# Kernel tuning notes

Measured on AMD Instinct MI355X. Metric: run time of the kernel, lower is better.

## Reference

```python
import jax, jax.numpy as jnp
import numpy as np

ALPHA = 32.0
RANK = 256
SCALE = ALPHA / RANK


def setup_inputs() -> dict:
    key = jax.random.key(0)
    k1, k2, k3, k4 = jax.random.split(key, 4)
    x = jax.random.normal(k1, (4, 2048, 4096), dtype=jnp.float32)
    A = jax.random.normal(k2, (256, 4096), dtype=jnp.float32)   # (rank, in)
    B = jax.random.normal(k3, (4096, 256), dtype=jnp.float32)   # (out, rank)
    d_A = jnp.ones((256,), dtype=jnp.float32)                    # init = ones (as in module)
    d_B = jax.random.normal(k4, (4096,), dtype=jnp.float32)      # perturbed for a nontrivial test
    return {"x": x, "A": A, "B": B, "d_A": d_A, "d_B": d_B}


def reference(x, A, B, d_A, d_B):
    # Effective weight: diag(d_B) @ B @ diag(d_A) @ A  -> (out, in)
    scaled_A = d_A[:, None] * A                 # (rank, in)
    BA = B @ scaled_A                            # (out, in)
    W_vera = d_B[:, None] * BA                   # (out, in)
    # out = x @ W_vera.T * scale  -> (..., out)
    return jnp.einsum('bsi,oi->bso', x, W_vera) * SCALE
```

## Files before the change

### kernel.cpp

```cpp
#include <hip/hip_runtime.h>
#include <hip/hip_bf16.h>


#define SCALE_F 0.125f
#define M_TOT 8192
#define K_IN 4096
#define RANK 256
#define N_OUT 4096
#define S_SPLIT 4
#define KC 1024

typedef __bf16 bf16_t;
typedef __bf16 bf16x8 __attribute__((ext_vector_type(8)));
typedef __bf16 bf16x4 __attribute__((ext_vector_type(4)));
typedef float f32x4 __attribute__((ext_vector_type(4)));

typedef __attribute__((address_space(3))) unsigned int lds_u32_t;
typedef const __attribute__((address_space(1))) unsigned int glob_u32_t;

__device__ __forceinline__ void async16(const void* g, void* l) {
    __builtin_amdgcn_global_load_lds((glob_u32_t*)g, (lds_u32_t*)l, 16, 0, 0);
}

__global__ __launch_bounds__(256) void conv_A(const float* __restrict__ A,
                                              const float* __restrict__ dA,
                                              bf16_t* __restrict__ Ab) {
    int idx = blockIdx.x * 256 + threadIdx.x;
    float4 v = ((const float4*)A)[idx];
    float s = dA[idx >> 10];
    bf16x4 o;
    o.x = (bf16_t)(v.x * s); o.y = (bf16_t)(v.y * s);
    o.z = (bf16_t)(v.z * s); o.w = (bf16_t)(v.w * s);
    ((bf16x4*)Ab)[idx] = o;
}

__global__ __launch_bounds__(256) void conv_B(const float* __restrict__ B,
                                              bf16_t* __restrict__ Bb) {
    int idx = blockIdx.x * 256 + threadIdx.x;
    float4 v = ((const float4*)B)[idx];
    bf16x4 o;
    o.x = (bf16_t)v.x; o.y = (bf16_t)v.y; o.z = (bf16_t)v.z; o.w = (bf16_t)v.w;
    ((bf16x4*)Bb)[idx] = o;
}

__global__ __launch_bounds__(256) void gemm1(const float* __restrict__ x,
                                             const bf16_t* __restrict__ Ab,
                                             bf16_t* __restrict__ part) {
    __shared__ float  sX[64 * 64];
    __shared__ bf16_t sA[128 * 64];
    const int tid = threadIdx.x;
    const int lane = tid & 63, wave = tid >> 6;
    const int wm = wave >> 1, wn = wave & 1;
    const int l15 = lane & 15, quad = lane >> 4;
    const int bm = blockIdx.x * 64;
    const int bn = blockIdx.y * 128;
    const int k0 = blockIdx.z * KC;

    f32x4 acc[2][4];
    const f32x4 zero = {0.f, 0.f, 0.f, 0.f};
    #pragma unroll
    for (int i = 0; i < 2; i++)
        #pragma unroll
        for (int j = 0; j < 4; j++) acc[i][j] = zero;

    for (int kt = 0; kt < KC; kt += 64) {
        #pragma unroll
        for (int c = 0; c < 4; c++) {
            int idx = c * 256 + tid;
            int m = idx >> 4, kc = (idx & 15) * 4;
            async16(&x[(size_t)(bm + m) * K_IN + k0 + kt + kc], &sX[idx * 4]);
        }
        #pragma unroll
        for (int c = 0; c < 4; c++) {
            int idx = c * 256 + tid;
            int n = idx >> 3, kc = (idx & 7) * 8;
            async16(&Ab[(size_t)(bn + n) * K_IN + k0 + kt + kc], &sA[idx * 8]);
        }
        __syncthreads();
        #pragma unroll
        for (int ks = 0; ks < 2; ks++) {
            bf16x8 af[2], bfr[4];
            #pragma unroll
            for (int i = 0; i < 2; i++) {
                const float* p = &sX[(wm * 32 + i * 16 + l15) * 64 + ks * 32 + quad * 8];
                f32x4 v0 = *(const f32x4*)p;
                f32x4 v1 = *(const f32x4*)(p + 4);
                bf16x8 t;
                t[0] = (bf16_t)v0[0]; t[1] = (bf16_t)v0[1];
                t[2] = (bf16_t)v0[2]; t[3] = (bf16_t)v0[3];
                t[4] = (bf16_t)v1[0]; t[5] = (bf16_t)v1[1];
                t[6] = (bf16_t)v1[2]; t[7] = (bf16_t)v1[3];
                af[i] = t;
            }
            #pragma unroll
            for (int j = 0; j < 4; j++)
                bfr[j] = *(const bf16x8*)&sA[(wn * 64 + j * 16 + l15) * 64 + ks * 32 + quad * 8];
            #pragma unroll
            for (int i = 0; i < 2; i++)
                #pragma unroll
                for (int j = 0; j < 4; j++)
                    acc[i][j] = __builtin_amdgcn_mfma_f32_16x16x32_bf16(af[i], bfr[j], acc[i][j], 0, 0, 0);
        }
        __syncthreads();
    }
    bf16_t* p = part + (size_t)blockIdx.z * M_TOT * RANK;
    #pragma unroll
    for (int i = 0; i < 2; i++) {
        #pragma unroll
        for (int j = 0; j < 4; j++) {
            int col = bn + wn * 64 + j * 16 + l15;
            #pragma unroll
            for (int r = 0; r < 4; r++) {
                int row = bm + wm * 32 + i * 16 + quad * 4 + r;
                p[(size_t)row * RANK + col] = (bf16_t)acc[i][j][r];
            }
        }
    }
}

__global__ __launch_bounds__(256) void reduce_t(const bf16_t* __restrict__ part,
                                                bf16_t* __restrict__ t) {
    int i = (blockIdx.x * 256 + threadIdx.x) * 8;
    float s[8] = {0.f, 0.f, 0.f, 0.f, 0.f, 0.f, 0.f, 0.f};
    #pragma unroll
    for (int z = 0; z < S_SPLIT; z++) {
        bf16x8 v = *(const bf16x8*)&part[(size_t)z * M_TOT * RANK + i];
        #pragma unroll
        for (int e = 0; e < 8; e++) s[e] += (float)v[e];
    }
    bf16x8 o;
    #pragma unroll
    for (int e = 0; e < 8; e++) o[e] = (bf16_t)s[e];
    *(bf16x8*)&t[i] = o;
}

__global__ __launch_bounds__(256) void gemm2(const bf16_t* __restrict__ t,
                                             const bf16_t* __restrict__ Bb,
                                             const float* __restrict__ dB,
                                             float* __restrict__ out) {
    __shared__ bf16_t sT[128 * 64];
    __shared__ bf16_t sB[64 * 64];
    const int tid = threadIdx.x;
    const int lane = tid & 63, wave = tid >> 6;
    const int wm = wave >> 1, wn = wave & 1;
    const int l15 = lane & 15, quad = lane >> 4;
    const int bm = blockIdx.x * 128;
    const int bn = blockIdx.y * 64;

    f32x4 acc[4][2];
    const f32x4 zero = {0.f, 0.f, 0.f, 0.f};
    #pragma unroll
    for (int i = 0; i < 4; i++)
        #pragma unroll
        for (int j = 0; j < 2; j++) acc[i][j] = zero;

    for (int kt = 0; kt < RANK; kt += 64) {
        #pragma unroll
        for (int c = 0; c < 4; c++) {
            int idx = c * 256 + tid;
            int m = idx >> 3, kc = (idx & 7) * 8;
            async16(&t[(size_t)(bm + m) * RANK + kt + kc], &sT[idx * 8]);
        }
        #pragma unroll
        for (int c = 0; c < 2; c++) {
            int idx = c * 256 + tid;
            int n = idx >> 3, kc = (idx & 7) * 8;
            async16(&Bb[(size_t)(bn + n) * RANK + kt + kc], &sB[idx * 8]);
        }
        __syncthreads();
        #pragma unroll
        for (int ks = 0; ks < 2; ks++) {
            bf16x8 af[4], bfr[2];
            #pragma unroll
            for (int i = 0; i < 4; i++)
                af[i] = *(const bf16x8*)&sT[(wm * 64 + i * 16 + l15) * 64 + ks * 32 + quad * 8];
            #pragma unroll
            for (int j = 0; j < 2; j++)
                bfr[j] = *(const bf16x8*)&sB[(wn * 32 + j * 16 + l15) * 64 + ks * 32 + quad * 8];
            #pragma unroll
            for (int i = 0; i < 4; i++)
                #pragma unroll
                for (int j = 0; j < 2; j++)
                    acc[i][j] = __builtin_amdgcn_mfma_f32_16x16x32_bf16(af[i], bfr[j], acc[i][j], 0, 0, 0);
        }
        __syncthreads();
    }
    #pragma unroll
    for (int j = 0; j < 2; j++) {
        int col = bn + wn * 32 + j * 16 + l15;
        float db = dB[col] * SCALE_F;
        #pragma unroll
        for (int i = 0; i < 4; i++) {
            #pragma unroll
            for (int r = 0; r < 4; r++) {
                int row = bm + wm * 64 + i * 16 + quad * 4 + r;
                out[(size_t)row * N_OUT + col] = db * acc[i][j][r];
            }
        }
    }
}

extern "C" void kernel_launch(void* const* d_in, const int* in_sizes, int n_in,
                              void* d_out, int out_size, void* d_ws, size_t ws_size,
                              hipStream_t stream) {
    const float* x  = (const float*)d_in[0];
    const float* A  = (const float*)d_in[1];
    const float* B  = (const float*)d_in[2];
    const float* dA = (const float*)d_in[3];
    const float* dB = (const float*)d_in[4];
    float* out = (float*)d_out;

    char* ws = (char*)d_ws;
    bf16_t* Ab   = (bf16_t*)ws;
    bf16_t* Bb   = (bf16_t*)(ws + (1u << 21));
    bf16_t* tt   = (bf16_t*)(ws + (1u << 22));
    bf16_t* part = (bf16_t*)(ws + (1u << 23));

    conv_A<<<1024, 256, 0, stream>>>(A, dA, Ab);
    conv_B<<<1024, 256, 0, stream>>>(B, Bb);
    gemm1<<<dim3(128, 2, S_SPLIT), 256, 0, stream>>>(x, Ab, part);
    reduce_t<<<1024, 256, 0, stream>>>(part, tt);
    gemm2<<<dim3(64, 64), 256, 0, stream>>>(tt, Bb, dB, out);
}
```

Measured before the change: 314.3 us.

## Retile both GEMMs with XOR-swizzled LDS, full-rank tiles, and merged conversion kernel

Merges the A and B fp32-to-bf16 conversion kernels into one launch. gemm1 now computes all 256 rank columns per block, so x is read from HBM once instead of twice, and it uses split-K 8 with K-step 32. gemm2 drops to 64x64 tiles for more blocks. Both kernels gain XOR swizzles on LDS to avoid bank conflicts. The trade-offs are a doubled partial-sum buffer and reduction traffic, plus higher register pressure in gemm1 with 16 accumulators.

Result: slower. 330.8 us (+5.3%).

```diff
diff --git a/kernel.cpp b/kernel.cpp
--- a/kernel.cpp
+++ b/kernel.cpp
@@ -7,8 +7,8 @@
 #define K_IN 4096
 #define RANK 256
 #define N_OUT 4096
-#define S_SPLIT 4
-#define KC 1024
+#define S_SPLIT 8
+#define KC 512
 
 typedef __bf16 bf16_t;
 typedef __bf16 bf16x8 __attribute__((ext_vector_type(8)));
@@ -22,97 +22,100 @@
     __builtin_amdgcn_global_load_lds((glob_u32_t*)g, (lds_u32_t*)l, 16, 0, 0);
 }
 
-__global__ __launch_bounds__(256) void conv_A(const float* __restrict__ A,
-                                              const float* __restrict__ dA,
-                                              bf16_t* __restrict__ Ab) {
-    int idx = blockIdx.x * 256 + threadIdx.x;
-    float4 v = ((const float4*)A)[idx];
-    float s = dA[idx >> 10];
-    bf16x4 o;
-    o.x = (bf16_t)(v.x * s); o.y = (bf16_t)(v.y * s);
-    o.z = (bf16_t)(v.z * s); o.w = (bf16_t)(v.w * s);
-    ((bf16x4*)Ab)[idx] = o;
-}
-
-__global__ __launch_bounds__(256) void conv_B(const float* __restrict__ B,
-                                              bf16_t* __restrict__ Bb) {
-    int idx = blockIdx.x * 256 + threadIdx.x;
-    float4 v = ((const float4*)B)[idx];
-    bf16x4 o;
-    o.x = (bf16_t)v.x; o.y = (bf16_t)v.y; o.z = (bf16_t)v.z; o.w = (bf16_t)v.w;
-    ((bf16x4*)Bb)[idx] = o;
+__global__ __launch_bounds__(256) void conv_AB(const float* __restrict__ A,
+                                               const float* __restrict__ dA,
+                                               const float* __restrict__ B,
+                                               bf16_t* __restrict__ Ab,
+                                               bf16_t* __restrict__ Bb) {
+    int b = blockIdx.x;
+    int idx = (b & 1023) * 256 + threadIdx.x;
+    if (b < 1024) {
+        float4 v = ((const float4*)A)[idx];
+        float s = dA[idx >> 10];
+        bf16x4 o;
+        o.x = (bf16_t)(v.x * s); o.y = (bf16_t)(v.y * s);
+        o.z = (bf16_t)(v.z * s); o.w = (bf16_t)(v.w * s);
+        ((bf16x4*)Ab)[idx] = o;
+    } else {
+        float4 v = ((const float4*)B)[idx];
+        bf16x4 o;
+        o.x = (bf16_t)v.x; o.y = (bf16_t)v.y; o.z = (bf16_t)v.z; o.w = (bf16_t)v.w;
+        ((bf16x4*)Bb)[idx] = o;
+    }
 }
 
 __global__ __launch_bounds__(256) void gemm1(const float* __restrict__ x,
                                              const bf16_t* __restrict__ Ab,
                                              bf16_t* __restrict__ part) {
-    __shared__ float  sX[64 * 64];
-    __shared__ bf16_t sA[128 * 64];
+    __shared__ float  sX[64 * 32];
+    __shared__ bf16_t sA[256 * 32];
     const int tid = threadIdx.x;
     const int lane = tid & 63, wave = tid >> 6;
     const int wm = wave >> 1, wn = wave & 1;
     const int l15 = lane & 15, quad = lane >> 4;
     const int bm = blockIdx.x * 64;
-    const int bn = blockIdx.y * 128;
-    const int k0 = blockIdx.z * KC;
-
-    f32x4 acc[2][4];
+    const int k0 = blockIdx.y * KC;
+
+    f32x4 acc[2][8];
     const f32x4 zero = {0.f, 0.f, 0.f, 0.f};
     #pragma unroll
     for (int i = 0; i < 2; i++)
         #pragma unroll
-        for (int j = 0; j < 4; j++) acc[i][j] = zero;
-
-    for (int kt = 0; kt < KC; kt += 64) {
+        for (int j = 0; j < 8; j++) acc[i][j] = zero;
+
+    for (int kt = 0; kt < KC; kt += 32) {
+        #pragma unroll
+        for (int c = 0; c < 2; c++) {
+            int u = c * 256 + tid;
+            int m = u >> 3, p = u & 7;
+            int kcu = p ^ (m & 7);
+            async16(&x[(size_t)(bm + m) * K_IN + k0 + kt + kcu * 4], &sX[u * 4]);
+        }
         #pragma unroll
         for (int c = 0; c < 4; c++) {
-            int idx = c * 256 + tid;
-            int m = idx >> 4, kc = (idx & 15) * 4;
-            async16(&x[(size_t)(bm + m) * K_IN + k0 + kt + kc], &sX[idx * 4]);
-        }
-        #pragma unroll
-        for (int c = 0; c < 4; c++) {
-            int idx = c * 256 + tid;
-            int n = idx >> 3, kc = (idx & 7) * 8;
-            async16(&Ab[(size_t)(bn + n) * K_IN + k0 + kt + kc], &sA[idx * 8]);
-        }
-        __syncthreads();
-        #pragma unroll
-        for (int ks = 0; ks < 2; ks++) {
-            bf16x8 af[2], bfr[4];
-            #pragma unroll
-            for (int i = 0; i < 2; i++) {
-                const float* p = &sX[(wm * 32 + i * 16 + l15) * 64 + ks * 32 + quad * 8];
-                f32x4 v0 = *(const f32x4*)p;
-                f32x4 v1 = *(const f32x4*)(p + 4);
-                bf16x8 t;
-                t[0] = (bf16_t)v0[0]; t[1] = (bf16_t)v0[1];
-                t[2] = (bf16_t)v0[2]; t[3] = (bf16_t)v0[3];
-                t[4] = (bf16_t)v1[0]; t[5] = (bf16_t)v1[1];
-                t[6] = (bf16_t)v1[2]; t[7] = (bf16_t)v1[3];
-                af[i] = t;
-            }
-            #pragma unroll
-            for (int j = 0; j < 4; j++)
-                bfr[j] = *(const bf16x8*)&sA[(wn * 64 + j * 16 + l15) * 64 + ks * 32 + quad * 8];
-            #pragma unroll
-            for (int i = 0; i < 2; i++)
-                #pragma unroll
-                for (int j = 0; j < 4; j++)
-                    acc[i][j] = __builtin_amdgcn_mfma_f32_16x16x32_bf16(af[i], bfr[j], acc[i][j], 0, 0, 0);
-        }
-        __syncthreads();
-    }
-    bf16_t* p = part + (size_t)blockIdx.z * M_TOT * RANK;
+            int u = c * 256 + tid;
+            int n = u >> 2, p = u & 3;
+            int kc8 = p ^ ((n >> 1) & 3);
+            async16(&Ab[(size_t)n * K_IN + k0 + kt + kc8 * 8], &sA[u * 8]);
+        }
+        __syncthreads();
+        bf16x8 af[2], bfr[8];
+        #pragma unroll
+        for (int i = 0; i < 2; i++) {
+            int m = wm * 32 + i * 16 + l15;
+            int p0 = (quad * 2) ^ (m & 7);
+            f32x4 v0 = *(const f32x4*)&sX[m * 32 + p0 * 4];
+            f32x4 v1 = *(const f32x4*)&sX[m * 32 + (p0 ^ 1) * 4];
+            bf16x8 t;
+            t[0] = (bf16_t)v0[0]; t[1] = (bf16_t)v0[1];
+            t[2] = (bf16_t)v0[2]; t[3] = (bf16_t)v0[3];
+            t[4] = (bf16_t)v1[0]; t[5] = (bf16_t)v1[1];
+            t[6] = (bf16_t)v1[2]; t[7] = (bf16_t)v1[3];
+            af[i] = t;
+        }
+        #pragma unroll
+        for (int j = 0; j < 8; j++) {
+            int n = wn * 128 + j * 16 + l15;
+            int p = quad ^ ((n >> 1) & 3);
+            bfr[j] = *(const bf16x8*)&sA[n * 32 + p * 8];
+        }
+        #pragma unroll
+        for (int i = 0; i < 2; i++)
+            #pragma unroll
+            for (int j = 0; j < 8; j++)
+                acc[i][j] = __builtin_amdgcn_mfma_f32_16x16x32_bf16(af[i], bfr[j], acc[i][j], 0, 0, 0);
+        __syncthreads();
+    }
+    bf16_t* pp = part + (size_t)blockIdx.y * M_TOT * RANK;
     #pragma unroll
     for (int i = 0; i < 2; i++) {
         #pragma unroll
-        for (int j = 0; j < 4; j++) {
-            int col = bn + wn * 64 + j * 16 + l15;
+        for (int j = 0; j < 8; j++) {
+            int col = wn * 128 + j * 16 + l15;
             #pragma unroll
             for (int r = 0; r < 4; r++) {
                 int row = bm + wm * 32 + i * 16 + quad * 4 + r;
-                p[(size_t)row * RANK + col] = (bf16_t)acc[i][j][r];
+                pp[(size_t)row * RANK + col] = (bf16_t)acc[i][j][r];
             }
         }
     }
@@ -138,47 +141,55 @@
                                              const bf16_t* __restrict__ Bb,
                                              const float* __restrict__ dB,
                                              float* __restrict__ out) {
-    __shared__ bf16_t sT[128 * 64];
+    __shared__ bf16_t sT[64 * 64];
     __shared__ bf16_t sB[64 * 64];
     const int tid = threadIdx.x;
     const int lane = tid & 63, wave = tid >> 6;
     const int wm = wave >> 1, wn = wave & 1;
     const int l15 = lane & 15, quad = lane >> 4;
-    const int bm = blockIdx.x * 128;
+    const int bm = blockIdx.x * 64;
     const int bn = blockIdx.y * 64;
 
-    f32x4 acc[4][2];
+    f32x4 acc[2][2];
     const f32x4 zero = {0.f, 0.f, 0.f, 0.f};
     #pragma unroll
-    for (int i = 0; i < 4; i++)
+    for (int i = 0; i < 2; i++)
         #pragma unroll
         for (int j = 0; j < 2; j++) acc[i][j] = zero;
 
     for (int kt = 0; kt < RANK; kt += 64) {
         #pragma unroll
-        for (int c = 0; c < 4; c++) {
-            int idx = c * 256 + tid;
-            int m = idx >> 3, kc = (idx & 7) * 8;
-            async16(&t[(size_t)(bm + m) * RANK + kt + kc], &sT[idx * 8]);
-        }
-        #pragma unroll
         for (int c = 0; c < 2; c++) {
-            int idx = c * 256 + tid;
-            int n = idx >> 3, kc = (idx & 7) * 8;
-            async16(&Bb[(size_t)(bn + n) * RANK + kt + kc], &sB[idx * 8]);
+            int u = c * 256 + tid;
+            int row = u >> 3, p = u & 7;
+            int kcu = p ^ (row & 7);
+            async16(&t[(size_t)(bm + row) * RANK + kt + kcu * 8], &sT[u * 8]);
+        }
+        #pragma unroll
+        for (int c = 0; c < 2; c++) {
+            int u = c * 256 + tid;
+            int row = u >> 3, p = u & 7;
+            int kcu = p ^ (row & 7);
+            async16(&Bb[(size_t)(bn + row) * RANK + kt + kcu * 8], &sB[u * 8]);
         }
         __syncthreads();
         #pragma unroll
         for (int ks = 0; ks < 2; ks++) {
-            bf16x8 af[4], bfr[2];
-            #pragma unroll
-            for (int i = 0; i < 4; i++)
-                af[i] = *(const bf16x8*)&sT[(wm * 64 + i * 16 + l15) * 64 + ks * 32 + quad * 8];
-            #pragma unroll
-            for (int j = 0; j < 2; j++)
-                bfr[j] = *(const bf16x8*)&sB[(wn * 32 + j * 16 + l15) * 64 + ks * 32 + quad * 8];
-            #pragma unroll
-            for (int i = 0; i < 4; i++)
+            bf16x8 af[2], bfr[2];
+            #pragma unroll
+            for (int i = 0; i < 2; i++) {
+                int row = wm * 32 + i * 16 + l15;
+                int p = (ks * 4 + quad) ^ (row & 7);
+                af[i] = *(const bf16x8*)&sT[row * 64 + p * 8];
+            }
+            #pragma unroll
+            for (int j = 0; j < 2; j++) {
+                int row = wn * 32 + j * 16 + l15;
+                int p = (ks * 4 + quad) ^ (row & 7);
+                bfr[j] = *(const bf16x8*)&sB[row * 64 + p * 8];
+            }
+            #pragma unroll
+            for (int i = 0; i < 2; i++)
                 #pragma unroll
                 for (int j = 0; j < 2; j++)
                     acc[i][j] = __builtin_amdgcn_mfma_f32_16x16x32_bf16(af[i], bfr[j], acc[i][j], 0, 0, 0);
@@ -190,10 +201,10 @@
         int col = bn + wn * 32 + j * 16 + l15;
         float db = dB[col] * SCALE_F;
         #pragma unroll
-        for (int i = 0; i < 4; i++) {
+        for (int i = 0; i < 2; i++) {
             #pragma unroll
             for (int r = 0; r < 4; r++) {
-                int row = bm + wm * 64 + i * 16 + quad * 4 + r;
+                int row = bm + wm * 32 + i * 16 + quad * 4 + r;
                 out[(size_t)row * N_OUT + col] = db * acc[i][j][r];
             }
         }
@@ -216,9 +227,8 @@
     bf16_t* tt   = (bf16_t*)(ws + (1u << 22));
     bf16_t* part = (bf16_t*)(ws + (1u << 23));
 
-    conv_A<<<1024, 256, 0, stream>>>(A, dA, Ab);
-    conv_B<<<1024, 256, 0, stream>>>(B, Bb);
-    gemm1<<<dim3(128, 2, S_SPLIT), 256, 0, stream>>>(x, Ab, part);
+    conv_AB<<<2048, 256, 0, stream>>>(A, dA, B, Ab, Bb);
+    gemm1<<<dim3(128, S_SPLIT), 256, 0, stream>>>(x, Ab, part);
     reduce_t<<<1024, 256, 0, stream>>>(part, tt);
-    gemm2<<<dim3(64, 64), 256, 0, stream>>>(tt, Bb, dB, out);
-}
+    gemm2<<<dim3(128, 64), 256, 0, stream>>>(tt, Bb, dB, out);
+}
```
